# Kernel optimization log

Measured on AMD Instinct MI355X. Metric: run time of the kernel, lower is better.

## Reference

```python
import jax, jax.numpy as jnp
import numpy as np

B, LC, LQ, D = 256, 400, 50, 128
NEG = 1e12


def setup_inputs() -> dict:
    key = jax.random.key(0)
    ks = jax.random.split(key, 7)
    return {
        "x_cont": jax.random.normal(ks[0], (B, LC, D), dtype=jnp.float32),
        "x_ques": jax.random.normal(ks[1], (B, LQ, D), dtype=jnp.float32),
        "W0": jax.random.normal(ks[2], (D, 1), dtype=jnp.float32) * (1.0 / np.sqrt(D)),
        "W1": jax.random.normal(ks[3], (D, 1), dtype=jnp.float32) * (1.0 / np.sqrt(D)),
        "W2": jax.random.normal(ks[4], (1, 1, D), dtype=jnp.float32) * (1.0 / np.sqrt(D)),
        "cont_len": jax.random.randint(ks[5], (B, 1), 1, LC, dtype=jnp.int32),
        "ques_len": jax.random.randint(ks[6], (B, 1), 1, LQ, dtype=jnp.int32),
    }


def reference(x_cont, x_ques, W0, W1, W2, cont_len, ques_len):
    # Trilinear similarity S[b,c,q] = xc.W0 + xq.W1 + (xc*W2).xq
    s_c = x_cont @ W0                                   # (B, LC, 1)
    s_q = jnp.swapaxes(x_ques @ W1, 1, 2)               # (B, 1, LQ)
    s_f = jnp.einsum('bcd,bqd->bcq', x_cont * W2, x_ques)
    S = s_c + s_q + s_f                                 # (B, LC, LQ)

    # Length masks: position valid iff pos < seq_len (matches one_hot+cumsum)
    q_mask = (jnp.arange(LQ)[None, :] < ques_len).astype(S.dtype)  # (B, LQ)
    c_mask = (jnp.arange(LC)[None, :] < cont_len).astype(S.dtype)  # (B, LC)

    S_bar = jax.nn.softmax(S - (1.0 - q_mask)[:, None, :] * NEG, axis=-1)
    S_T = jnp.swapaxes(
        jax.nn.softmax(S - (1.0 - c_mask)[:, :, None] * NEG, axis=1), 1, 2)  # (B, LQ, LC)

    c2q = S_bar @ x_ques                                # (B, LC, D)
    q2c = (S_bar @ S_T) @ x_cont                        # (B, LC, D)

    result = jnp.concatenate(
        [x_cont, c2q, x_cont * c2q, x_cont * q2c], axis=-1)  # (B, LC, 4D)
    return result, S_bar, S_T
```

## Files before the change

kernel.cpp:

```cpp
#include <hip/hip_runtime.h>
#include <math.h>

#define B 256
#define LC 400
#define LQ 50
#define D 128
#define CT 64

__global__ __launch_bounds__(256) void k_scores_rowsm(
    const float* __restrict__ xc_g, const float* __restrict__ xq_g,
    const float* __restrict__ W0, const float* __restrict__ W1,
    const float* __restrict__ W2, const int* __restrict__ ques_len,
    float* __restrict__ S_bar, float* __restrict__ S_Traw)
{
    __shared__ __align__(16) float xq[56 * 132];
    __shared__ __align__(16) float xc[CT * 132];
    __shared__ float w[3 * D];
    __shared__ float sq[56], sc[CT];
    __shared__ float sS[CT * 51];
    __shared__ float rowm[CT], rowi[CT];

    const int b = blockIdx.y;
    const int c0 = blockIdx.x * CT;
    const int t = threadIdx.x;
    const int nc = min(CT, LC - c0);
    const int qlen = ques_len[b];

    const float4* xq4g = (const float4*)(xq_g + (size_t)b * LQ * D);
    for (int i = t; i < LQ * 32; i += 256)
        ((float4*)xq)[(i >> 5) * 33 + (i & 31)] = xq4g[i];
    const float4* xc4g = (const float4*)(xc_g + (size_t)(b * LC + c0) * D);
    for (int i = t; i < nc * 32; i += 256)
        ((float4*)xc)[(i >> 5) * 33 + (i & 31)] = xc4g[i];
    if (t < D) { w[t] = W0[t]; w[D + t] = W1[t]; w[2 * D + t] = W2[t]; }
    __syncthreads();

    if (t < LQ) {
        const float4* r = (const float4*)(xq + t * 132);
        const float4* wv = (const float4*)(w + D);
        float4 a = {0.f, 0.f, 0.f, 0.f};
#pragma unroll
        for (int d = 0; d < 32; ++d) {
            float4 u = r[d], v = wv[d];
            a.x += u.x * v.x; a.y += u.y * v.y; a.z += u.z * v.z; a.w += u.w * v.w;
        }
        sq[t] = a.x + a.y + a.z + a.w;
    } else if (t >= 64 && t < 64 + CT) {
        const int c = t - 64;
        if (c < nc) {
            const float4* r = (const float4*)(xc + c * 132);
            const float4* wv = (const float4*)w;
            float4 a = {0.f, 0.f, 0.f, 0.f};
#pragma unroll
            for (int d = 0; d < 32; ++d) {
                float4 u = r[d], v = wv[d];
                a.x += u.x * v.x; a.y += u.y * v.y; a.z += u.z * v.z; a.w += u.w * v.w;
            }
            sc[c] = a.x + a.y + a.z + a.w;
        }
    }
    __syncthreads();
    for (int i = t; i < LQ * D; i += 256)
        xq[(i >> 7) * 132 + (i & 127)] *= w[2 * D + (i & 127)];
    __syncthreads();

    const int qg = t & 7, cg = t >> 3;
    const int cA = cg * 2;
    if (cA < nc) {
        float accA[7] = {0, 0, 0, 0, 0, 0, 0};
        float accB[7] = {0, 0, 0, 0, 0, 0, 0};
        const float4* xc4 = (const float4*)xc;
        const float4* xq4 = (const float4*)xq;
#pragma unroll 8
        for (int d4 = 0; d4 < 32; ++d4) {
            const float4 a0 = xc4[cA * 33 + d4];
            const float4 a1 = xc4[(cA + 1) * 33 + d4];
#pragma unroll
            for (int j = 0; j < 7; ++j) {
                const float4 bq = xq4[(qg * 7 + j) * 33 + d4];
                accA[j] += a0.x * bq.x + a0.y * bq.y + a0.z * bq.z + a0.w * bq.w;
                accB[j] += a1.x * bq.x + a1.y * bq.y + a1.z * bq.z + a1.w * bq.w;
            }
        }
        const float scA = sc[cA], scB = sc[cA + 1];
#pragma unroll
        for (int j = 0; j < 7; ++j) {
            const int q = qg * 7 + j;
            if (q < LQ) {
                sS[cA * 51 + q] = accA[j] + scA + sq[q];
                sS[(cA + 1) * 51 + q] = accB[j] + scB + sq[q];
            }
        }
    }
    __syncthreads();

    if (t < nc) {
        float m = -INFINITY;
        for (int q = 0; q < qlen; ++q) m = fmaxf(m, sS[t * 51 + q]);
        float s = 0.f;
        for (int q = 0; q < qlen; ++q) s += __expf(sS[t * 51 + q] - m);
        rowm[t] = m;
        rowi[t] = 1.f / s;
    }
    __syncthreads();

    float* Sb = S_bar + (size_t)(b * LC + c0) * LQ;
    for (int i = t; i < nc * LQ; i += 256) {
        const int c = i / LQ, q = i - c * LQ;
        Sb[i] = (q < qlen) ? __expf(sS[c * 51 + q] - rowm[c]) * rowi[c] : 0.f;
    }
    float* STb = S_Traw + (size_t)b * LQ * LC + c0;
    for (int i = t; i < LQ * 64; i += 256) {
        const int q = i >> 6, c = i & 63;
        if (c < nc) STb[q * LC + c] = sS[c * 51 + q];
    }
}

__global__ __launch_bounds__(512) void k_colsm_qc(
    float* __restrict__ S_T, const float* __restrict__ xc_g,
    const int* __restrict__ cont_len, float* __restrict__ T)
{
    __shared__ __align__(16) float sT[56 * 404];
    __shared__ float red[256];
    __shared__ float colmax[LQ], colinv[LQ];

    const int b = blockIdx.x;
    const int t = threadIdx.x;
    const int clen = cont_len[b];
    float* STb = S_T + (size_t)b * LQ * LC;

    const float4* STb4 = (const float4*)STb;
    float4* sTw = (float4*)sT;
    for (int i = t; i < LQ * 100; i += 512)
        sTw[(i / 100) * 101 + (i % 100)] = STb4[i];
    __syncthreads();

    const int qr = t / 5, g = t - qr * 5;
    if (t < 250) {
        float m = -INFINITY;
        const int ce = min((g + 1) * 80, clen);
        for (int c = g * 80; c < ce; ++c) m = fmaxf(m, sT[qr * 404 + c]);
        red[t] = m;
    }
    __syncthreads();
    if (t < LQ) {
        float m = red[t * 5];
#pragma unroll
        for (int k = 1; k < 5; ++k) m = fmaxf(m, red[t * 5 + k]);
        colmax[t] = m;
    }
    __syncthreads();
    if (t < 250) {
        float s = 0.f;
        const float cm = colmax[qr];
        const int ce = min((g + 1) * 80, clen);
        for (int c = g * 80; c < ce; ++c) s += __expf(sT[qr * 404 + c] - cm);
        red[t] = s;
    }
    __syncthreads();
    if (t < LQ) {
        float s = red[t * 5];
#pragma unroll
        for (int k = 1; k < 5; ++k) s += red[t * 5 + k];
        colinv[t] = 1.f / s;
    }
    __syncthreads();

    for (int i = t; i < LQ * LC; i += 512) {
        const int q = i / LC, c = i - q * LC;
        const float v = (c < clen) ? __expf(sT[q * 404 + c] - colmax[q]) * colinv[q] : 0.f;
        sT[q * 404 + c] = v;
        STb[i] = v;
    }
    __syncthreads();

    const int d4 = t & 31, qg = t >> 5;
    const int qb = qg * 4;
    float4 acc[4];
#pragma unroll
    for (int j = 0; j < 4; ++j) acc[j] = make_float4(0.f, 0.f, 0.f, 0.f);

    const float4* xcv = (const float4*)xc_g + (size_t)b * LC * 32 + d4;
    const float4* sT4 = (const float4*)sT;
    for (int c = 0; c < LC; c += 4) {
        const float4 x0 = xcv[(c + 0) * 32];
        const float4 x1 = xcv[(c + 1) * 32];
        const float4 x2 = xcv[(c + 2) * 32];
        const float4 x3 = xcv[(c + 3) * 32];
#pragma unroll
        for (int j = 0; j < 4; ++j) {
            const int q = min(qb + j, LQ - 1);
            const float4 wv = sT4[q * 101 + (c >> 2)];
            acc[j].x += wv.x * x0.x + wv.y * x1.x + wv.z * x2.x + wv.w * x3.x;
            acc[j].y += wv.x * x0.y + wv.y * x1.y + wv.z * x2.y + wv.w * x3.y;
            acc[j].z += wv.x * x0.z + wv.y * x1.z + wv.z * x2.z + wv.w * x3.z;
            acc[j].w += wv.x * x0.w + wv.y * x1.w + wv.z * x2.w + wv.w * x3.w;
        }
    }
    float4* Tb = (float4*)T + (size_t)b * LQ * 32 + d4;
#pragma unroll
    for (int j = 0; j < 4; ++j) {
        const int q = qb + j;
        if (q < LQ) Tb[q * 32] = acc[j];
    }
}

#define FMA4(A, s, V) { A.x += (s) * V.x; A.y += (s) * V.y; A.z += (s) * V.z; A.w += (s) * V.w; }

__global__ __launch_bounds__(256) void k_out(
    const float* __restrict__ S_bar, const float* __restrict__ xq_g,
    const float* __restrict__ Tm, const float* __restrict__ xc_g,
    float* __restrict__ out)
{
    __shared__ __align__(16) float xqL[LQ * 132];
    __shared__ __align__(16) float TL[LQ * 132];
    __shared__ __align__(16) float sbT[LQ * 68];

    const int b = blockIdx.y;
    const int c0 = blockIdx.x * CT;
    const int t = threadIdx.x;
    const int nc = min(CT, LC - c0);

    const float4* xq4g = (const float4*)(xq_g + (size_t)b * LQ * D);
    const float4* T4g  = (const float4*)(Tm + (size_t)b * LQ * D);
    for (int i = t; i < LQ * 32; i += 256) {
        const int row = i >> 5, col = i & 31;
        ((float4*)xqL)[row * 33 + col] = xq4g[i];
        ((float4*)TL)[row * 33 + col]  = T4g[i];
    }
    const float* sb_g = S_bar + (size_t)(b * LC + c0) * LQ;
    for (int i = t; i < nc * LQ; i += 256) {
        const int c = i / LQ, q = i - c * LQ;
        sbT[q * 68 + c] = sb_g[i];
    }
    __syncthreads();

    const int d4 = t & 31, cg = t >> 5;
    float4 c2q[8], q2c[8];
#pragma unroll
    for (int i = 0; i < 8; ++i) {
        c2q[i] = make_float4(0.f, 0.f, 0.f, 0.f);
        q2c[i] = make_float4(0.f, 0.f, 0.f, 0.f);
    }
    const float4* xq4 = (const float4*)xqL;
    const float4* T4  = (const float4*)TL;
    const float4* sb4 = (const float4*)sbT;
    const int cb2 = cg * 2;
    for (int qq = 0; qq < LQ; ++qq) {
        const float4 xv = xq4[qq * 33 + d4];
        const float4 tv = T4[qq * 33 + d4];
        const float4 s0 = sb4[qq * 17 + cb2];
        const float4 s1 = sb4[qq * 17 + cb2 + 1];
        FMA4(c2q[0], s0.x, xv); FMA4(q2c[0], s0.x, tv);
        FMA4(c2q[1], s0.y, xv); FMA4(q2c[1], s0.y, tv);
        FMA4(c2q[2], s0.z, xv); FMA4(q2c[2], s0.z, tv);
        FMA4(c2q[3], s0.w, xv); FMA4(q2c[3], s0.w, tv);
        FMA4(c2q[4], s1.x, xv); FMA4(q2c[4], s1.x, tv);
        FMA4(c2q[5], s1.y, xv); FMA4(q2c[5], s1.y, tv);
        FMA4(c2q[6], s1.z, xv); FMA4(q2c[6], s1.z, tv);
        FMA4(c2q[7], s1.w, xv); FMA4(q2c[7], s1.w, tv);
    }

    const int cbase = cg * 8;
    const float4* xcv = (const float4*)xc_g;
    float4* out4 = (float4*)out;
#pragma unroll
    for (int i = 0; i < 8; ++i) {
        const int c = cbase + i;
        if (c < nc) {
            const int row = b * LC + c0 + c;
            const float4 xc = xcv[(size_t)row * 32 + d4];
            float4* o = out4 + (size_t)row * 128 + d4;
            o[0] = xc;
            o[32] = c2q[i];
            o[64] = make_float4(xc.x * c2q[i].x, xc.y * c2q[i].y,
                                xc.z * c2q[i].z, xc.w * c2q[i].w);
            o[96] = make_float4(xc.x * q2c[i].x, xc.y * q2c[i].y,
                                xc.z * q2c[i].z, xc.w * q2c[i].w);
        }
    }
}

extern "C" void kernel_launch(void* const* d_in, const int* in_sizes, int n_in,
                              void* d_out, int out_size, void* d_ws, size_t ws_size,
                              hipStream_t stream)
{
    (void)in_sizes; (void)n_in; (void)out_size; (void)ws_size;
    const float* x_cont = (const float*)d_in[0];
    const float* x_ques = (const float*)d_in[1];
    const float* W0 = (const float*)d_in[2];
    const float* W1 = (const float*)d_in[3];
    const float* W2 = (const float*)d_in[4];
    const int* cont_len = (const int*)d_in[5];
    const int* ques_len = (const int*)d_in[6];

    float* out = (float*)d_out;
    float* out_res  = out;
    float* out_Sbar = out + (size_t)B * LC * 4 * D;
    float* out_ST   = out_Sbar + (size_t)B * LC * LQ;
    float* Tws = (float*)d_ws;

    k_scores_rowsm<<<dim3(7, B), 256, 0, stream>>>(x_cont, x_ques, W0, W1, W2,
                                                   ques_len, out_Sbar, out_ST);
    k_colsm_qc<<<B, 512, 0, stream>>>(out_ST, x_cont, cont_len, Tws);
    k_out<<<dim3(7, B), 256, 0, stream>>>(out_Sbar, x_ques, Tws, x_cont, out_res);
}
```

Before: 446.7 us.

## Split column softmax across query halves and widen thread parallelism in output kernel

The column-softmax/q2c kernel now runs two blocks per batch, each owning 25 query rows, which halves its shared memory and doubles the grid. The output kernel moves to 512 threads with 4 context rows per thread and prefetches x_cont rows before the accumulation loop. The scores kernel restructures its register tile to 4 strided context rows per thread using only 128 threads, and zero-pads the extra query rows. Launch-bound occupancy hints are added. The split means each q-half block rereads x_cont, and fewer threads in the scores GEMM may lower its throughput.

```diff
diff --git a/kernel.cpp b/kernel.cpp
--- a/kernel.cpp
+++ b/kernel.cpp
@@ -7,7 +7,7 @@
 #define D 128
 #define CT 64
 
-__global__ __launch_bounds__(256) void k_scores_rowsm(
+__global__ __launch_bounds__(256, 2) void k_scores_rowsm(
     const float* __restrict__ xc_g, const float* __restrict__ xq_g,
     const float* __restrict__ W0, const float* __restrict__ W1,
     const float* __restrict__ W2, const int* __restrict__ ques_len,
@@ -16,7 +16,7 @@
     __shared__ __align__(16) float xq[56 * 132];
     __shared__ __align__(16) float xc[CT * 132];
     __shared__ float w[3 * D];
-    __shared__ float sq[56], sc[CT];
+    __shared__ float sq[52], sc[CT];
     __shared__ float sS[CT * 51];
     __shared__ float rowm[CT], rowi[CT];
 
@@ -27,8 +27,10 @@
     const int qlen = ques_len[b];
 
     const float4* xq4g = (const float4*)(xq_g + (size_t)b * LQ * D);
-    for (int i = t; i < LQ * 32; i += 256)
-        ((float4*)xq)[(i >> 5) * 33 + (i & 31)] = xq4g[i];
+    for (int i = t; i < 56 * 32; i += 256) {
+        float4 v = (i < LQ * 32) ? xq4g[i] : make_float4(0.f, 0.f, 0.f, 0.f);
+        ((float4*)xq)[(i >> 5) * 33 + (i & 31)] = v;
+    }
     const float4* xc4g = (const float4*)(xc_g + (size_t)(b * LC + c0) * D);
     for (int i = t; i < nc * 32; i += 256)
         ((float4*)xc)[(i >> 5) * 33 + (i & 31)] = xc4g[i];
@@ -45,7 +47,7 @@
             a.x += u.x * v.x; a.y += u.y * v.y; a.z += u.z * v.z; a.w += u.w * v.w;
         }
         sq[t] = a.x + a.y + a.z + a.w;
-    } else if (t >= 64 && t < 64 + CT) {
+    } else if (t >= 64 && t < 128) {
         const int c = t - 64;
         if (c < nc) {
             const float4* r = (const float4*)(xc + c * 132);
@@ -64,31 +66,40 @@
         xq[(i >> 7) * 132 + (i & 127)] *= w[2 * D + (i & 127)];
     __syncthreads();
 
-    const int qg = t & 7, cg = t >> 3;
-    const int cA = cg * 2;
-    if (cA < nc) {
-        float accA[7] = {0, 0, 0, 0, 0, 0, 0};
-        float accB[7] = {0, 0, 0, 0, 0, 0, 0};
+    if (t < 128) {
+        const int qg = t & 7, cg = t >> 3;
+        float acc[4][7];
+#pragma unroll
+        for (int k = 0; k < 4; ++k)
+#pragma unroll
+            for (int j = 0; j < 7; ++j) acc[k][j] = 0.f;
         const float4* xc4 = (const float4*)xc;
         const float4* xq4 = (const float4*)xq;
-#pragma unroll 8
+#pragma unroll 4
         for (int d4 = 0; d4 < 32; ++d4) {
-            const float4 a0 = xc4[cA * 33 + d4];
-            const float4 a1 = xc4[(cA + 1) * 33 + d4];
+            const float4 a0 = xc4[(cg + 0)  * 33 + d4];
+            const float4 a1 = xc4[(cg + 16) * 33 + d4];
+            const float4 a2 = xc4[(cg + 32) * 33 + d4];
+            const float4 a3 = xc4[(cg + 48) * 33 + d4];
 #pragma unroll
             for (int j = 0; j < 7; ++j) {
                 const float4 bq = xq4[(qg * 7 + j) * 33 + d4];
-                accA[j] += a0.x * bq.x + a0.y * bq.y + a0.z * bq.z + a0.w * bq.w;
-                accB[j] += a1.x * bq.x + a1.y * bq.y + a1.z * bq.z + a1.w * bq.w;
+                acc[0][j] += a0.x*bq.x + a0.y*bq.y + a0.z*bq.z + a0.w*bq.w;
+                acc[1][j] += a1.x*bq.x + a1.y*bq.y + a1.z*bq.z + a1.w*bq.w;
+                acc[2][j] += a2.x*bq.x + a2.y*bq.y + a2.z*bq.z + a2.w*bq.w;
+                acc[3][j] += a3.x*bq.x + a3.y*bq.y + a3.z*bq.z + a3.w*bq.w;
             }
         }
-        const float scA = sc[cA], scB = sc[cA + 1];
-#pragma unroll
-        for (int j = 0; j < 7; ++j) {
-            const int q = qg * 7 + j;
-            if (q < LQ) {
-                sS[cA * 51 + q] = accA[j] + scA + sq[q];
-                sS[(cA + 1) * 51 + q] = accB[j] + scB + sq[q];
+#pragma unroll
+        for (int k = 0; k < 4; ++k) {
+            const int c = cg + 16 * k;
+            if (c < nc) {
+                const float scc = sc[c];
+#pragma unroll
+                for (int j = 0; j < 7; ++j) {
+                    const int q = qg * 7 + j;
+                    if (q < LQ) sS[c * 51 + q] = acc[k][j] + scc + sq[q];
+                }
             }
         }
     }
@@ -116,57 +127,59 @@
     }
 }
 
-__global__ __launch_bounds__(512) void k_colsm_qc(
+__global__ __launch_bounds__(512, 4) void k_colsm_qc(
     float* __restrict__ S_T, const float* __restrict__ xc_g,
     const int* __restrict__ cont_len, float* __restrict__ T)
 {
-    __shared__ __align__(16) float sT[56 * 404];
+    __shared__ __align__(16) float sT[25 * 404];
     __shared__ float red[256];
-    __shared__ float colmax[LQ], colinv[LQ];
-
-    const int b = blockIdx.x;
+    __shared__ float colmax[28], colinv[28];
+
+    const int half = blockIdx.x;
+    const int b = blockIdx.y;
+    const int q0 = half * 25;
     const int t = threadIdx.x;
     const int clen = cont_len[b];
-    float* STb = S_T + (size_t)b * LQ * LC;
+    float* STb = S_T + ((size_t)b * LQ + q0) * LC;
 
     const float4* STb4 = (const float4*)STb;
     float4* sTw = (float4*)sT;
-    for (int i = t; i < LQ * 100; i += 512)
+    for (int i = t; i < 25 * 100; i += 512)
         sTw[(i / 100) * 101 + (i % 100)] = STb4[i];
     __syncthreads();
 
-    const int qr = t / 5, g = t - qr * 5;
+    const int qr = t / 10, g = t - qr * 10;
     if (t < 250) {
         float m = -INFINITY;
-        const int ce = min((g + 1) * 80, clen);
-        for (int c = g * 80; c < ce; ++c) m = fmaxf(m, sT[qr * 404 + c]);
+        const int ce = min((g + 1) * 40, clen);
+        for (int c = g * 40; c < ce; ++c) m = fmaxf(m, sT[qr * 404 + c]);
         red[t] = m;
     }
     __syncthreads();
-    if (t < LQ) {
-        float m = red[t * 5];
-#pragma unroll
-        for (int k = 1; k < 5; ++k) m = fmaxf(m, red[t * 5 + k]);
+    if (t < 25) {
+        float m = red[t * 10];
+#pragma unroll
+        for (int k = 1; k < 10; ++k) m = fmaxf(m, red[t * 10 + k]);
         colmax[t] = m;
     }
     __syncthreads();
     if (t < 250) {
         float s = 0.f;
         const float cm = colmax[qr];
-        const int ce = min((g + 1) * 80, clen);
-        for (int c = g * 80; c < ce; ++c) s += __expf(sT[qr * 404 + c] - cm);
+        const int ce = min((g + 1) * 40, clen);
+        for (int c = g * 40; c < ce; ++c) s += __expf(sT[qr * 404 + c] - cm);
         red[t] = s;
     }
     __syncthreads();
-    if (t < LQ) {
-        float s = red[t * 5];
-#pragma unroll
-        for (int k = 1; k < 5; ++k) s += red[t * 5 + k];
+    if (t < 25) {
+        float s = red[t * 10];
+#pragma unroll
+        for (int k = 1; k < 10; ++k) s += red[t * 10 + k];
         colinv[t] = 1.f / s;
     }
     __syncthreads();
 
-    for (int i = t; i < LQ * LC; i += 512) {
+    for (int i = t; i < 25 * LC; i += 512) {
         const int q = i / LC, c = i - q * LC;
         const float v = (c < clen) ? __expf(sT[q * 404 + c] - colmax[q]) * colinv[q] : 0.f;
         sT[q * 404 + c] = v;
@@ -175,10 +188,9 @@
     __syncthreads();
 
     const int d4 = t & 31, qg = t >> 5;
-    const int qb = qg * 4;
-    float4 acc[4];
-#pragma unroll
-    for (int j = 0; j < 4; ++j) acc[j] = make_float4(0.f, 0.f, 0.f, 0.f);
+    float4 acc0 = make_float4(0.f, 0.f, 0.f, 0.f);
+    float4 acc1 = make_float4(0.f, 0.f, 0.f, 0.f);
+    const bool has1 = (qg + 16) < 25;
 
     const float4* xcv = (const float4*)xc_g + (size_t)b * LC * 32 + d4;
     const float4* sT4 = (const float4*)sT;
@@ -187,27 +199,29 @@
         const float4 x1 = xcv[(c + 1) * 32];
         const float4 x2 = xcv[(c + 2) * 32];
         const float4 x3 = xcv[(c + 3) * 32];
-#pragma unroll
-        for (int j = 0; j < 4; ++j) {
-            const int q = min(qb + j, LQ - 1);
-            const float4 wv = sT4[q * 101 + (c >> 2)];
-            acc[j].x += wv.x * x0.x + wv.y * x1.x + wv.z * x2.x + wv.w * x3.x;
-            acc[j].y += wv.x * x0.y + wv.y * x1.y + wv.z * x2.y + wv.w * x3.y;
-            acc[j].z += wv.x * x0.z + wv.y * x1.z + wv.z * x2.z + wv.w * x3.z;
-            acc[j].w += wv.x * x0.w + wv.y * x1.w + wv.z * x2.w + wv.w * x3.w;
+        {
+            const float4 wv = sT4[qg * 101 + (c >> 2)];
+            acc0.x += wv.x * x0.x + wv.y * x1.x + wv.z * x2.x + wv.w * x3.x;
+            acc0.y += wv.x * x0.y + wv.y * x1.y + wv.z * x2.y + wv.w * x3.y;
+            acc0.z += wv.x * x0.z + wv.y * x1.z + wv.z * x2.z + wv.w * x3.z;
+            acc0.w += wv.x * x0.w + wv.y * x1.w + wv.z * x2.w + wv.w * x3.w;
+        }
+        if (has1) {
+            const float4 wv = sT4[(qg + 16) * 101 + (c >> 2)];
+            acc1.x += wv.x * x0.x + wv.y * x1.x + wv.z * x2.x + wv.w * x3.x;
+            acc1.y += wv.x * x0.y + wv.y * x1.y + wv.z * x2.y + wv.w * x3.y;
+            acc1.z += wv.x * x0.z + wv.y * x1.z + wv.z * x2.z + wv.w * x3.z;
+            acc1.w += wv.x * x0.w + wv.y * x1.w + wv.z * x2.w + wv.w * x3.w;
         }
     }
     float4* Tb = (float4*)T + (size_t)b * LQ * 32 + d4;
-#pragma unroll
-    for (int j = 0; j < 4; ++j) {
-        const int q = qb + j;
-        if (q < LQ) Tb[q * 32] = acc[j];
-    }
+    Tb[(q0 + qg) * 32] = acc0;
+    if (has1) Tb[(q0 + qg + 16) * 32] = acc1;
 }
 
 #define FMA4(A, s, V) { A.x += (s) * V.x; A.y += (s) * V.y; A.z += (s) * V.z; A.w += (s) * V.w; }
 
-__global__ __launch_bounds__(256) void k_out(
+__global__ __launch_bounds__(512, 4) void k_out(
     const float* __restrict__ S_bar, const float* __restrict__ xq_g,
     const float* __restrict__ Tm, const float* __restrict__ xc_g,
     float* __restrict__ out)
@@ -223,53 +237,56 @@
 
     const float4* xq4g = (const float4*)(xq_g + (size_t)b * LQ * D);
     const float4* T4g  = (const float4*)(Tm + (size_t)b * LQ * D);
-    for (int i = t; i < LQ * 32; i += 256) {
+    for (int i = t; i < LQ * 32; i += 512) {
         const int row = i >> 5, col = i & 31;
         ((float4*)xqL)[row * 33 + col] = xq4g[i];
         ((float4*)TL)[row * 33 + col]  = T4g[i];
     }
     const float* sb_g = S_bar + (size_t)(b * LC + c0) * LQ;
-    for (int i = t; i < nc * LQ; i += 256) {
+    for (int i = t; i < CT * LQ; i += 512) {
         const int c = i / LQ, q = i - c * LQ;
-        sbT[q * 68 + c] = sb_g[i];
+        sbT[q * 68 + c] = (c < nc) ? sb_g[i] : 0.f;
     }
     __syncthreads();
 
     const int d4 = t & 31, cg = t >> 5;
-    float4 c2q[8], q2c[8];
-#pragma unroll
-    for (int i = 0; i < 8; ++i) {
+    const int cbase = cg * 4;
+
+    const float4* xcv = (const float4*)xc_g;
+    float4 xcr[4];
+#pragma unroll
+    for (int i = 0; i < 4; ++i) {
+        int row = b * LC + c0 + cbase + i;
+        row = min(row, B * LC - 1);
+        xcr[i] = xcv[(size_t)row * 32 + d4];
+    }
+
+    float4 c2q[4], q2c[4];
+#pragma unroll
+    for (int i = 0; i < 4; ++i) {
         c2q[i] = make_float4(0.f, 0.f, 0.f, 0.f);
         q2c[i] = make_float4(0.f, 0.f, 0.f, 0.f);
     }
     const float4* xq4 = (const float4*)xqL;
     const float4* T4  = (const float4*)TL;
     const float4* sb4 = (const float4*)sbT;
-    const int cb2 = cg * 2;
     for (int qq = 0; qq < LQ; ++qq) {
         const float4 xv = xq4[qq * 33 + d4];
         const float4 tv = T4[qq * 33 + d4];
-        const float4 s0 = sb4[qq * 17 + cb2];
-        const float4 s1 = sb4[qq * 17 + cb2 + 1];
+        const float4 s0 = sb4[qq * 17 + cg];
         FMA4(c2q[0], s0.x, xv); FMA4(q2c[0], s0.x, tv);
         FMA4(c2q[1], s0.y, xv); FMA4(q2c[1], s0.y, tv);
         FMA4(c2q[2], s0.z, xv); FMA4(q2c[2], s0.z, tv);
         FMA4(c2q[3], s0.w, xv); FMA4(q2c[3], s0.w, tv);
-        FMA4(c2q[4], s1.x, xv); FMA4(q2c[4], s1.x, tv);
-        FMA4(c2q[5], s1.y, xv); FMA4(q2c[5], s1.y, tv);
-        FMA4(c2q[6], s1.z, xv); FMA4(q2c[6], s1.z, tv);
-        FMA4(c2q[7], s1.w, xv); FMA4(q2c[7], s1.w, tv);
-    }
-
-    const int cbase = cg * 8;
-    const float4* xcv = (const float4*)xc_g;
+    }
+
     float4* out4 = (float4*)out;
 #pragma unroll
-    for (int i = 0; i < 8; ++i) {
+    for (int i = 0; i < 4; ++i) {
         const int c = cbase + i;
         if (c < nc) {
             const int row = b * LC + c0 + c;
-            const float4 xc = xcv[(size_t)row * 32 + d4];
+            const float4 xc = xcr[i];
             float4* o = out4 + (size_t)row * 128 + d4;
             o[0] = xc;
             o[32] = c2q[i];
@@ -302,6 +319,6 @@
 
     k_scores_rowsm<<<dim3(7, B), 256, 0, stream>>>(x_cont, x_ques, W0, W1, W2,
                                                    ques_len, out_Sbar, out_ST);
-    k_colsm_qc<<<B, 512, 0, stream>>>(out_ST, x_cont, cont_len, Tws);
-    k_out<<<dim3(7, B), 256, 0, stream>>>(out_Sbar, x_ques, Tws, x_cont, out_res);
+    k_colsm_qc<<<dim3(2, B), 512, 0, stream>>>(out_ST, x_cont, cont_len, Tws);
+    k_out<<<dim3(7, B), 512, 0, stream>>>(out_Sbar, x_ques, Tws, x_cont, out_res);
 }
```

After: 475.3 us. 6.4% more time.

## Split score dot products across thread halves and prefetch x_cont in output kernel

Applied to the files above, without the earlier changes.

The score kernel now gives every thread four context rows and half of the D dimension. Two thread halves each compute partial sums, which are combined through shared memory with an extra barrier, so all 256 threads work instead of only those with valid row pairs. The output kernel loads its x_cont rows into registers before the shared-memory barrier to hide global latency, and both kernels gain a minimum-occupancy launch bound of 2. The cost is more registers per thread, an extra sync, and zero-padding of the shared tiles.

```diff
diff --git a/kernel.cpp b/kernel.cpp
--- a/kernel.cpp
+++ b/kernel.cpp
@@ -7,7 +7,7 @@
 #define D 128
 #define CT 64
 
-__global__ __launch_bounds__(256) void k_scores_rowsm(
+__global__ __launch_bounds__(256, 2) void k_scores_rowsm(
     const float* __restrict__ xc_g, const float* __restrict__ xq_g,
     const float* __restrict__ W0, const float* __restrict__ W1,
     const float* __restrict__ W2, const int* __restrict__ ques_len,
@@ -27,8 +27,10 @@
     const int qlen = ques_len[b];
 
     const float4* xq4g = (const float4*)(xq_g + (size_t)b * LQ * D);
-    for (int i = t; i < LQ * 32; i += 256)
-        ((float4*)xq)[(i >> 5) * 33 + (i & 31)] = xq4g[i];
+    for (int i = t; i < 56 * 32; i += 256) {
+        float4 v = (i < LQ * 32) ? xq4g[i] : make_float4(0.f, 0.f, 0.f, 0.f);
+        ((float4*)xq)[(i >> 5) * 33 + (i & 31)] = v;
+    }
     const float4* xc4g = (const float4*)(xc_g + (size_t)(b * LC + c0) * D);
     for (int i = t; i < nc * 32; i += 256)
         ((float4*)xc)[(i >> 5) * 33 + (i & 31)] = xc4g[i];
@@ -45,7 +47,7 @@
             a.x += u.x * v.x; a.y += u.y * v.y; a.z += u.z * v.z; a.w += u.w * v.w;
         }
         sq[t] = a.x + a.y + a.z + a.w;
-    } else if (t >= 64 && t < 64 + CT) {
+    } else if (t >= 64 && t < 128) {
         const int c = t - 64;
         if (c < nc) {
             const float4* r = (const float4*)(xc + c * 132);
@@ -64,31 +66,63 @@
         xq[(i >> 7) * 132 + (i & 127)] *= w[2 * D + (i & 127)];
     __syncthreads();
 
-    const int qg = t & 7, cg = t >> 3;
-    const int cA = cg * 2;
-    if (cA < nc) {
-        float accA[7] = {0, 0, 0, 0, 0, 0, 0};
-        float accB[7] = {0, 0, 0, 0, 0, 0, 0};
+    const int qg = t & 7;
+    const int cg = (t >> 3) & 15;
+    const int half = t >> 7;
+    const int d0 = half * 16;
+
+    float acc[4][7];
+#pragma unroll
+    for (int k = 0; k < 4; ++k)
+#pragma unroll
+        for (int j = 0; j < 7; ++j) acc[k][j] = 0.f;
+
+    {
         const float4* xc4 = (const float4*)xc;
         const float4* xq4 = (const float4*)xq;
-#pragma unroll 8
-        for (int d4 = 0; d4 < 32; ++d4) {
-            const float4 a0 = xc4[cA * 33 + d4];
-            const float4 a1 = xc4[(cA + 1) * 33 + d4];
+#pragma unroll 4
+        for (int dd = 0; dd < 16; ++dd) {
+            const int d4 = d0 + dd;
+            const float4 a0 = xc4[(cg + 0)  * 33 + d4];
+            const float4 a1 = xc4[(cg + 16) * 33 + d4];
+            const float4 a2 = xc4[(cg + 32) * 33 + d4];
+            const float4 a3 = xc4[(cg + 48) * 33 + d4];
 #pragma unroll
             for (int j = 0; j < 7; ++j) {
                 const float4 bq = xq4[(qg * 7 + j) * 33 + d4];
-                accA[j] += a0.x * bq.x + a0.y * bq.y + a0.z * bq.z + a0.w * bq.w;
-                accB[j] += a1.x * bq.x + a1.y * bq.y + a1.z * bq.z + a1.w * bq.w;
+                acc[0][j] += a0.x*bq.x + a0.y*bq.y + a0.z*bq.z + a0.w*bq.w;
+                acc[1][j] += a1.x*bq.x + a1.y*bq.y + a1.z*bq.z + a1.w*bq.w;
+                acc[2][j] += a2.x*bq.x + a2.y*bq.y + a2.z*bq.z + a2.w*bq.w;
+                acc[3][j] += a3.x*bq.x + a3.y*bq.y + a3.z*bq.z + a3.w*bq.w;
             }
         }
-        const float scA = sc[cA], scB = sc[cA + 1];
-#pragma unroll
-        for (int j = 0; j < 7; ++j) {
-            const int q = qg * 7 + j;
-            if (q < LQ) {
-                sS[cA * 51 + q] = accA[j] + scA + sq[q];
-                sS[(cA + 1) * 51 + q] = accB[j] + scB + sq[q];
+    }
+    if (half) {
+#pragma unroll
+        for (int k = 0; k < 4; ++k) {
+            const int c = cg + 16 * k;
+            if (c < nc) {
+#pragma unroll
+                for (int j = 0; j < 7; ++j) {
+                    const int q = qg * 7 + j;
+                    if (q < LQ) sS[c * 51 + q] = acc[k][j];
+                }
+            }
+        }
+    }
+    __syncthreads();
+    if (!half) {
+#pragma unroll
+        for (int k = 0; k < 4; ++k) {
+            const int c = cg + 16 * k;
+            if (c < nc) {
+                const float scc = sc[c];
+#pragma unroll
+                for (int j = 0; j < 7; ++j) {
+                    const int q = qg * 7 + j;
+                    if (q < LQ)
+                        sS[c * 51 + q] = acc[k][j] + sS[c * 51 + q] + scc + sq[q];
+                }
             }
         }
     }
@@ -207,7 +241,7 @@
 
 #define FMA4(A, s, V) { A.x += (s) * V.x; A.y += (s) * V.y; A.z += (s) * V.z; A.w += (s) * V.w; }
 
-__global__ __launch_bounds__(256) void k_out(
+__global__ __launch_bounds__(256, 2) void k_out(
     const float* __restrict__ S_bar, const float* __restrict__ xq_g,
     const float* __restrict__ Tm, const float* __restrict__ xc_g,
     float* __restrict__ out)
@@ -229,13 +263,24 @@
         ((float4*)TL)[row * 33 + col]  = T4g[i];
     }
     const float* sb_g = S_bar + (size_t)(b * LC + c0) * LQ;
-    for (int i = t; i < nc * LQ; i += 256) {
+    for (int i = t; i < CT * LQ; i += 256) {
         const int c = i / LQ, q = i - c * LQ;
-        sbT[q * 68 + c] = sb_g[i];
-    }
-    __syncthreads();
+        sbT[q * 68 + c] = (c < nc) ? sb_g[i] : 0.f;
+    }
 
     const int d4 = t & 31, cg = t >> 5;
+    const int cbase = cg * 8;
+
+    const float4* xcv = (const float4*)xc_g;
+    float4 xcr[8];
+#pragma unroll
+    for (int i = 0; i < 8; ++i) {
+        int row = b * LC + c0 + cbase + i;
+        row = min(row, B * LC - 1);
+        xcr[i] = xcv[(size_t)row * 32 + d4];
+    }
+    __syncthreads();
+
     float4 c2q[8], q2c[8];
 #pragma unroll
     for (int i = 0; i < 8; ++i) {
@@ -261,15 +306,13 @@
         FMA4(c2q[7], s1.w, xv); FMA4(q2c[7], s1.w, tv);
     }
 
-    const int cbase = cg * 8;
-    const float4* xcv = (const float4*)xc_g;
     float4* out4 = (float4*)out;
 #pragma unroll
     for (int i = 0; i < 8; ++i) {
         const int c = cbase + i;
         if (c < nc) {
             const int row = b * LC + c0 + c;
-            const float4 xc = xcv[(size_t)row * 32 + d4];
+            const float4 xc = xcr[i];
             float4* o = out4 + (size_t)row * 128 + d4;
             o[0] = xc;
             o[32] = c2q[i];
```

After: 439.8 us. Within noise of the previous version (-1.5%).
